# Kernel tuning notes

Hardware: AMD Instinct MI355X
Metric: run time of the kernel (lower is better)

## Reference

```python
import jax, jax.numpy as jnp
import numpy as np

B, T, N, F_IN, F_OUT, H = 32, 32, 256, 32, 32, 256
NEG_SLOPE = 0.2  # GATConv default leaky-relu slope


def setup_inputs() -> dict:
    key = jax.random.key(0)
    ks = jax.random.split(key, 12)
    x = jax.random.normal(ks[0], (B, T, N, F_IN), dtype=jnp.float32)
    u = jax.random.uniform(ks[1], (B, T, N, N))
    w = jax.random.uniform(ks[2], (B, T, N, N))
    adj = jnp.where(u < 0.1, w, 0.0).astype(jnp.float32)
    # GAT params (heads=1, concat=False)
    W = jax.random.normal(ks[3], (F_IN, F_OUT), dtype=jnp.float32) / np.sqrt(F_IN)
    a_src = jax.random.normal(ks[4], (F_OUT,), dtype=jnp.float32) / np.sqrt(F_OUT)
    a_dst = jax.random.normal(ks[5], (F_OUT,), dtype=jnp.float32) / np.sqrt(F_OUT)
    gat_b = jnp.zeros((F_OUT,), dtype=jnp.float32)
    # LSTM params (PyTorch layout, gate order i,f,g,o)
    IN = N * F_OUT
    s = 1.0 / np.sqrt(H)
    W_ih = jax.random.uniform(ks[6], (4 * H, IN), minval=-s, maxval=s, dtype=jnp.float32)
    W_hh = jax.random.uniform(ks[7], (4 * H, H), minval=-s, maxval=s, dtype=jnp.float32)
    b_ih = jax.random.uniform(ks[8], (4 * H,), minval=-s, maxval=s, dtype=jnp.float32)
    b_hh = jax.random.uniform(ks[9], (4 * H,), minval=-s, maxval=s, dtype=jnp.float32)
    # output Linear
    Wo = jax.random.uniform(ks[10], (N, H), minval=-s, maxval=s, dtype=jnp.float32)
    bo = jax.random.uniform(ks[11], (N,), minval=-s, maxval=s, dtype=jnp.float32)
    return {"x": x, "adj": adj, "W": W, "a_src": a_src, "a_dst": a_dst,
            "gat_b": gat_b, "W_ih": W_ih, "W_hh": W_hh, "b_ih": b_ih,
            "b_hh": b_hh, "Wo": Wo, "bo": bo}


def _gat(x, adj, W, a_src, a_dst, gat_b):
    # batched over (B,T). h: [B,T,N,F_OUT]
    h = jnp.einsum('btnf,fo->btno', x, W)
    s_src = jnp.einsum('btno,o->btn', h, a_src)  # contribution of source node j
    s_dst = jnp.einsum('btno,o->btn', h, a_dst)  # contribution of target node i
    # e[i,j] = LeakyReLU(a_dst.h_i + a_src.h_j)
    e = jax.nn.leaky_relu(s_dst[..., :, None] + s_src[..., None, :], NEG_SLOPE)
    # edge (row=j -> col=i) exists iff adj[j,i] != 0; GATConv adds self-loops
    mask = (jnp.swapaxes(adj, -1, -2) != 0) | jnp.eye(N, dtype=bool)
    alpha = jax.nn.softmax(jnp.where(mask, e, -jnp.inf), axis=-1)  # softmax over sources j per target i
    return jnp.einsum('btij,btjo->btio', alpha, h) + gat_b


def _lstm_last(seq, W_ih, W_hh, b_ih, b_hh):
    # seq: [B,T,IN] -> last hidden state [B,H]
    def step(carry, x_t):
        h_prev, c_prev = carry
        gates = x_t @ W_ih.T + h_prev @ W_hh.T + (b_ih + b_hh)
        i, f, g, o = jnp.split(gates, 4, axis=-1)
        c = jax.nn.sigmoid(f) * c_prev + jax.nn.sigmoid(i) * jnp.tanh(g)
        h = jax.nn.sigmoid(o) * jnp.tanh(c)
        return (h, c), None
    init = (jnp.zeros((seq.shape[0], H), seq.dtype), jnp.zeros((seq.shape[0], H), seq.dtype))
    (h_last, _), _ = jax.lax.scan(step, init, jnp.swapaxes(seq, 0, 1))
    return h_last


def reference(x, adj, W, a_src, a_dst, gat_b, W_ih, W_hh, b_ih, b_hh, Wo, bo):
    gat_out = _gat(x, adj, W, a_src, a_dst, gat_b)            # [B,T,N,F_OUT]
    seq = gat_out.reshape(gat_out.shape[0], gat_out.shape[1], -1)  # [B,T,N*F_OUT]
    h_last = _lstm_last(seq, W_ih, W_hh, b_ih, b_hh)          # [B,H]
    return h_last @ Wo.T + bo                                  # [B,N]
```

## Files before the change

### kernel.cpp

```cpp
#include <hip/hip_runtime.h>
#include <cstdint>

constexpr int B_ = 32, T_ = 32, N_ = 256, FIN = 32, FOUT = 32, H_ = 256;
constexpr int IN_ = N_ * FOUT;
constexpr int G4  = 4 * H_;
constexpr int BT  = B_ * T_;
#define NEG_SLOPE 0.2f

typedef _Float16 half8 __attribute__((ext_vector_type(8)));
typedef _Float16 h2    __attribute__((ext_vector_type(2)));
typedef float    f4    __attribute__((ext_vector_type(4)));

union U48 { uint4 u; half8 h; };

__device__ inline uint32_t pkh2(float a, float b) {
    union { uint32_t u; _Float16 h[2]; } z;
    z.h[0] = (_Float16)a; z.h[1] = (_Float16)b; return z.u;
}
__device__ inline float f16lo(uint32_t u){ union{uint32_t u; _Float16 h[2];} z; z.u=u; return (float)z.h[0]; }
__device__ inline float f16hi(uint32_t u){ union{uint32_t u; _Float16 h[2];} z; z.u=u; return (float)z.h[1]; }

__device__ inline float dot2f(uint32_t w, uint32_t h, float acc) {
    union { uint32_t u; h2 v; } a, b; a.u = w; b.u = h;
#if __has_builtin(__builtin_amdgcn_fdot2)
    return __builtin_amdgcn_fdot2(a.v, b.v, acc, false);
#else
    return acc + (float)a.v.x * (float)b.v.x + (float)a.v.y * (float)b.v.y;
#endif
}

__device__ inline void gload16(const void* g, void* l) {
    __builtin_amdgcn_global_load_lds(
        (const __attribute__((address_space(1))) void*)g,
        (__attribute__((address_space(3))) void*)l, 16, 0, 0);
}

__global__ __launch_bounds__(256) void gat_kernel(
    const float* __restrict__ x, const float* __restrict__ adj,
    const float* __restrict__ W, const float* __restrict__ a_src,
    const float* __restrict__ a_dst, const float* __restrict__ gat_b,
    _Float16* __restrict__ seq)
{
    const int bt = blockIdx.x;
    const int i  = threadIdx.x;
    const int L  = i & 63, w = i >> 6;
    __shared__ float Ws[FIN * FOUT];
    __shared__ __align__(16) _Float16 hT[32 * 264];
    __shared__ __align__(16) uint32_t Pc[256 * 36];
    __shared__ float ssrc[N_];
    __shared__ float linv[N_];
    __shared__ float asv[FOUT], adv[FOUT], gbv[FOUT];

    for (int t = i; t < FIN * FOUT; t += 256) Ws[t] = W[t];
    if (i < FOUT) { asv[i] = a_src[i]; adv[i] = a_dst[i]; gbv[i] = gat_b[i]; }

    float xr[FIN];
    const float* xrow = x + ((size_t)bt * N_ + i) * FIN;
    #pragma unroll
    for (int f4i = 0; f4i < FIN / 4; ++f4i) {
        float4 v = reinterpret_cast<const float4*>(xrow)[f4i];
        xr[4*f4i] = v.x; xr[4*f4i+1] = v.y; xr[4*f4i+2] = v.z; xr[4*f4i+3] = v.w;
    }
    __syncthreads();

    float hr[FOUT];
    #pragma unroll
    for (int k4 = 0; k4 < FOUT / 4; ++k4) {
        float ax = 0.f, ay = 0.f, az = 0.f, aw = 0.f;
        #pragma unroll
        for (int f = 0; f < FIN; ++f) {
            float4 w4 = *reinterpret_cast<const float4*>(&Ws[f*FOUT + 4*k4]);
            ax += xr[f]*w4.x; ay += xr[f]*w4.y; az += xr[f]*w4.z; aw += xr[f]*w4.w;
        }
        hr[4*k4] = ax; hr[4*k4+1] = ay; hr[4*k4+2] = az; hr[4*k4+3] = aw;
    }
    float ss = 0.f, sd = 0.f;
    #pragma unroll
    for (int k = 0; k < FOUT; ++k) { ss += hr[k]*asv[k]; sd += hr[k]*adv[k]; }
    #pragma unroll
    for (int k = 0; k < FOUT; ++k) hT[k*264 + i] = (_Float16)hr[k];
    ssrc[i] = ss;
    __syncthreads();

    float l = 0.f;
    f4 acc[4][2] = {};
    const float* adjcol = adj + (size_t)bt * N_ * N_ + i;
    const int key = (i >> 3) & 3;
    const int m = L & 15, G = L >> 4;

    for (int c = 0; c < 4; ++c) {
        const int j0 = c * 64;
        #pragma unroll 8
        for (int q = 0; q < 32; ++q) {
            int ja = j0 + 2*q, jb = ja + 1;
            float a0 = adjcol[(size_t)ja * N_];
            float a1 = adjcol[(size_t)jb * N_];
            float e0 = sd + ssrc[ja]; e0 = e0 > 0.f ? e0 : NEG_SLOPE * e0;
            float e1 = sd + ssrc[jb]; e1 = e1 > 0.f ? e1 : NEG_SLOPE * e1;
            float p0 = ((a0 != 0.f) || (ja == i)) ? __expf(e0) : 0.f;
            float p1 = ((a1 != 0.f) || (jb == i)) ? __expf(e1) : 0.f;
            l += p0 + p1;
            Pc[i*36 + (((q >> 2) ^ key) << 2) + (q & 3)] = pkh2(p0, p1);
        }
        #pragma unroll
        for (int ks = 0; ks < 2; ++ks) {
            U48 b0, b1;
            b0.h = *reinterpret_cast<const half8*>(&hT[m*264        + j0 + ks*32 + G*8]);
            b1.h = *reinterpret_cast<const half8*>(&hT[(m+16)*264   + j0 + ks*32 + G*8]);
            #pragma unroll
            for (int it = 0; it < 4; ++it) {
                int row = w*64 + it*16 + m;
                int rkey = (row >> 3) & 3;
                U48 a;
                a.u = reinterpret_cast<const uint4*>(&Pc[row*36])[ks*4 + (G ^ rkey)];
                acc[it][0] = __builtin_amdgcn_mfma_f32_16x16x32_f16(a.h, b0.h, acc[it][0], 0, 0, 0);
                acc[it][1] = __builtin_amdgcn_mfma_f32_16x16x32_f16(a.h, b1.h, acc[it][1], 0, 0, 0);
            }
        }
    }
    linv[i] = 1.f / l;
    _Float16* obase = seq + (size_t)bt * IN_;
    #pragma unroll
    for (int it = 0; it < 4; ++it) {
        int ib = w*64 + it*16 + G*4;
        #pragma unroll
        for (int ot = 0; ot < 2; ++ot) {
            int o = ot*16 + m;
            float gb = gbv[o];
            #pragma unroll
            for (int r = 0; r < 4; ++r) {
                int row = ib + r;
                obase[row * FOUT + o] = (_Float16)(acc[it][ot][r] * linv[row] + gb);
            }
        }
    }
}

__global__ __launch_bounds__(256) void pack_wih_kernel(
    const float* __restrict__ Wih, _Float16* __restrict__ out)
{
    int idx = (blockIdx.x * 256 + threadIdx.x) * 8;
    float4 v0 = *reinterpret_cast<const float4*>(Wih + idx);
    float4 v1 = *reinterpret_cast<const float4*>(Wih + idx + 4);
    half8 o;
    o[0]=(_Float16)v0.x; o[1]=(_Float16)v0.y; o[2]=(_Float16)v0.z; o[3]=(_Float16)v0.w;
    o[4]=(_Float16)v1.x; o[5]=(_Float16)v1.y; o[6]=(_Float16)v1.z; o[7]=(_Float16)v1.w;
    *reinterpret_cast<half8*>(out + idx) = o;
}

__global__ __launch_bounds__(256) void pack_whh_kernel(
    const float* __restrict__ Whh, uint32_t* __restrict__ pwv,
    uint32_t* __restrict__ pwl, uint32_t* __restrict__ pws)
{
    int g = blockIdx.x * 256 + threadIdx.x;
    const float* row = Whh + (size_t)g * H_;
    #pragma unroll
    for (int p = 0; p < 128; ++p) {
        float2 v = *reinterpret_cast<const float2*>(row + 2*p);
        uint32_t u = pkh2(v.x, v.y);
        if (p < 64) pwv[p * 1024 + g] = u;
        else if (p < 96) { int pp = p - 64; pwl[(pp >> 2) * 4096 + g * 4 + (pp & 3)] = u; }
        else             { int pp = p - 96; pws[(pp >> 2) * 4096 + g * 4 + (pp & 3)] = u; }
    }
}

__global__ __launch_bounds__(256, 4) void gemm_kernel(
    const _Float16* __restrict__ A, const _Float16* __restrict__ Bh,
    float* __restrict__ G)
{
    __shared__ __align__(16) _Float16 As[128 * 32];
    __shared__ __align__(16) _Float16 Bs[128 * 32];
    const int t = threadIdx.x;
    const int L = t & 63, w = t >> 6;
    const int wm = w & 1, wn = w >> 1;
    const int m0 = blockIdx.y * 128, n0 = blockIdx.x * 128;
    const int kz = blockIdx.z * 1024;

    f4 acc[4][4] = {};
    const int q0 = t, q1 = t + 256;
    const int row0 = q0 >> 2, kc0 = q0 & 3;
    const int row1 = q1 >> 2, kc1 = q1 & 3;
    const int la = (L & 15) * 32 + (L >> 4) * 8;

    const _Float16* A0 = A + (size_t)(m0 + row0) * IN_ + kz + kc0 * 8;
    const _Float16* A1 = A + (size_t)(m0 + row1) * IN_ + kz + kc1 * 8;
    const _Float16* B0 = Bh + (size_t)(n0 + row0) * IN_ + kz + kc0 * 8;
    const _Float16* B1 = Bh + (size_t)(n0 + row1) * IN_ + kz + kc1 * 8;
    for (int kb = 0; kb < 1024; kb += 32) {
        __syncthreads();
        gload16(A0 + kb, &As[q0 * 8]);
        gload16(A1 + kb, &As[q1 * 8]);
        gload16(B0 + kb, &Bs[q0 * 8]);
        gload16(B1 + kb, &Bs[q1 * 8]);
        __syncthreads();
        half8 af[4], bf[4];
        #pragma unroll
        for (int mi = 0; mi < 4; ++mi)
            af[mi] = *reinterpret_cast<const half8*>(&As[(wm*64 + mi*16) * 32 + la]);
        #pragma unroll
        for (int ni = 0; ni < 4; ++ni)
            bf[ni] = *reinterpret_cast<const half8*>(&Bs[(wn*64 + ni*16) * 32 + la]);
        #pragma unroll
        for (int mi = 0; mi < 4; ++mi)
            #pragma unroll
            for (int ni = 0; ni < 4; ++ni)
                acc[mi][ni] = __builtin_amdgcn_mfma_f32_16x16x32_f16(
                    af[mi], bf[ni], acc[mi][ni], 0, 0, 0);
    }
    const int cn = n0 + wn * 64 + (L & 15);
    const int rm = m0 + wm * 64 + (L >> 4) * 4;
    #pragma unroll
    for (int mi = 0; mi < 4; ++mi)
        #pragma unroll
        for (int ni = 0; ni < 4; ++ni)
            #pragma unroll
            for (int r = 0; r < 4; ++r)
                atomicAdd(&G[(size_t)(rm + mi*16 + r) * G4 + cn + ni*16], acc[mi][ni][r]);
}

__global__ __launch_bounds__(1024) void lstm_kernel(
    const float* __restrict__ G, const uint32_t* __restrict__ pwv,
    const uint32_t* __restrict__ pwl, const uint32_t* __restrict__ pws,
    const float* __restrict__ b_ih, const float* __restrict__ b_hh,
    const float* __restrict__ Wo, const float* __restrict__ bo,
    float* __restrict__ out)
{
    const int b = blockIdx.x;
    const int g = threadIdx.x;
    __shared__ __align__(16) uint32_t hsp[128];
    __shared__ float gsh[G4];
    __shared__ __align__(16) uint32_t wl[8 * 4096];

    uint32_t wv[64];
    #pragma unroll
    for (int p = 0; p < 64; ++p) wv[p] = pwv[p * 1024 + g];
    {
        const uint4* s = reinterpret_cast<const uint4*>(pwl);
        uint4* d = reinterpret_cast<uint4*>(wl);
        #pragma unroll
        for (int r = 0; r < 8; ++r) d[r * 1024 + g] = s[r * 1024 + g];
    }
    if (g < 128) hsp[g] = 0u;
    float c = 0.f;
    const float bias = b_ih[g] + b_hh[g];
    const float* Gb = G + (size_t)b * T_ * G4 + g;
    const uint4* pws4 = reinterpret_cast<const uint4*>(pws);
    const uint4* wl4  = reinterpret_cast<const uint4*>(wl);
    const uint4* hsp4 = reinterpret_cast<const uint4*>(hsp);
    float gnext = Gb[0];
    __syncthreads();

    for (int t = 0; t < T_; ++t) {
        float acc = bias + gnext;
        if (t + 1 < T_) gnext = Gb[(size_t)(t + 1) * G4];
        #pragma unroll
        for (int q = 0; q < 32; ++q) {
            uint4 h4 = hsp4[q];
            uint4 w4;
            if (q < 16) {
                w4.x = wv[4*q]; w4.y = wv[4*q+1]; w4.z = wv[4*q+2]; w4.w = wv[4*q+3];
            } else if (q < 24) {
                w4 = wl4[(q - 16) * 1024 + g];
            } else {
                w4 = pws4[(q - 24) * 1024 + g];
            }
            acc = dot2f(w4.x, h4.x, acc);
            acc = dot2f(w4.y, h4.y, acc);
            acc = dot2f(w4.z, h4.z, acc);
            acc = dot2f(w4.w, h4.w, acc);
        }
        gsh[g] = acc;
        __syncthreads();
        if (g < H_) {
            float xi = gsh[g], xf = gsh[H_ + g], xg = gsh[2*H_ + g], xo = gsh[3*H_ + g];
            float si = 1.f / (1.f + __expf(-xi));
            float sf = 1.f / (1.f + __expf(-xf));
            float so = 1.f / (1.f + __expf(-xo));
            float eg = __expf(2.f * xg);
            float tg = 1.f - 2.f / (eg + 1.f);
            c = sf * c + si * tg;
            float ec = __expf(2.f * c);
            float th = 1.f - 2.f / (ec + 1.f);
            reinterpret_cast<_Float16*>(hsp)[g] = (_Float16)(so * th);
        }
        __syncthreads();
    }
    if (g < N_) {
        const float* worow = Wo + (size_t)g * H_;
        float o = bo[g];
        #pragma unroll
        for (int q = 0; q < 32; ++q) {
            uint4 hq = hsp4[q];
            float4 w0 = *reinterpret_cast<const float4*>(worow + q*8);
            float4 w1 = *reinterpret_cast<const float4*>(worow + q*8 + 4);
            o += w0.x * f16lo(hq.x) + w0.y * f16hi(hq.x)
               + w0.z * f16lo(hq.y) + w0.w * f16hi(hq.y)
               + w1.x * f16lo(hq.z) + w1.y * f16hi(hq.z)
               + w1.z * f16lo(hq.w) + w1.w * f16hi(hq.w);
        }
        out[(size_t)b * N_ + g] = o;
    }
}

extern "C" void kernel_launch(void* const* d_in, const int* in_sizes, int n_in,
                              void* d_out, int out_size, void* d_ws, size_t ws_size,
                              hipStream_t stream) {
    const float* x     = (const float*)d_in[0];
    const float* adj   = (const float*)d_in[1];
    const float* W     = (const float*)d_in[2];
    const float* a_src = (const float*)d_in[3];
    const float* a_dst = (const float*)d_in[4];
    const float* gat_b = (const float*)d_in[5];
    const float* W_ih  = (const float*)d_in[6];
    const float* W_hh  = (const float*)d_in[7];
    const float* b_ih  = (const float*)d_in[8];
    const float* b_hh  = (const float*)d_in[9];
    const float* Wo    = (const float*)d_in[10];
    const float* bo    = (const float*)d_in[11];
    float* out = (float*)d_out;

    _Float16* seq   = (_Float16*)d_ws;
    _Float16* wih_h = seq + (size_t)BT * IN_;
    float*    G     = (float*)(wih_h + (size_t)G4 * IN_);
    uint32_t* pwv   = (uint32_t*)(G + (size_t)BT * G4);
    uint32_t* pwl   = pwv + 64 * 1024;
    uint32_t* pws   = pwl + 32 * 1024;

    hipMemsetAsync(G, 0, (size_t)BT * G4 * sizeof(float), stream);
    pack_whh_kernel<<<dim3(4), dim3(256), 0, stream>>>(W_hh, pwv, pwl, pws);
    pack_wih_kernel<<<dim3(4096), dim3(256), 0, stream>>>(W_ih, wih_h);
    gat_kernel<<<dim3(BT), dim3(256), 0, stream>>>(x, adj, W, a_src, a_dst, gat_b, seq);
    gemm_kernel<<<dim3(8, 8, 8), dim3(256), 0, stream>>>(seq, wih_h, G);
    lstm_kernel<<<dim3(B_), dim3(1024), 0, stream>>>(G, pwv, pwl, pws, b_ih, b_hh, Wo, bo, out);
}
```

Measured before the change: 585.0 us.

## Replace split-K atomics with partial buffers reduced in LSTM; merge pack kernels

Each split-K slice of the input-projection GEMM now writes its own partial buffer instead of doing atomicAdd into one shared buffer. The LSTM kernel sums the eight partials while it prefetches the next timestep's gates. This removes the memset and the atomic traffic. The two weight-packing kernels are merged into one launch. The cost is eight times the workspace for the partials and more global reads inside the serial LSTM loop.

```diff
diff --git a/kernel.cpp b/kernel.cpp
--- a/kernel.cpp
+++ b/kernel.cpp
@@ -5,6 +5,7 @@
 constexpr int IN_ = N_ * FOUT;
 constexpr int G4  = 4 * H_;
 constexpr int BT  = B_ * T_;
+constexpr int KZ  = 8;
 #define NEG_SLOPE 0.2f
 
 typedef _Float16 half8 __attribute__((ext_vector_type(8)));
@@ -105,8 +106,8 @@
         #pragma unroll
         for (int ks = 0; ks < 2; ++ks) {
             U48 b0, b1;
-            b0.h = *reinterpret_cast<const half8*>(&hT[m*264        + j0 + ks*32 + G*8]);
-            b1.h = *reinterpret_cast<const half8*>(&hT[(m+16)*264   + j0 + ks*32 + G*8]);
+            b0.h = *reinterpret_cast<const half8*>(&hT[m*264      + j0 + ks*32 + G*8]);
+            b1.h = *reinterpret_cast<const half8*>(&hT[(m+16)*264 + j0 + ks*32 + G*8]);
             #pragma unroll
             for (int it = 0; it < 4; ++it) {
                 int row = w*64 + it*16 + m;
@@ -136,37 +137,36 @@
     }
 }
 
-__global__ __launch_bounds__(256) void pack_wih_kernel(
-    const float* __restrict__ Wih, _Float16* __restrict__ out)
-{
-    int idx = (blockIdx.x * 256 + threadIdx.x) * 8;
-    float4 v0 = *reinterpret_cast<const float4*>(Wih + idx);
-    float4 v1 = *reinterpret_cast<const float4*>(Wih + idx + 4);
-    half8 o;
-    o[0]=(_Float16)v0.x; o[1]=(_Float16)v0.y; o[2]=(_Float16)v0.z; o[3]=(_Float16)v0.w;
-    o[4]=(_Float16)v1.x; o[5]=(_Float16)v1.y; o[6]=(_Float16)v1.z; o[7]=(_Float16)v1.w;
-    *reinterpret_cast<half8*>(out + idx) = o;
-}
-
-__global__ __launch_bounds__(256) void pack_whh_kernel(
-    const float* __restrict__ Whh, uint32_t* __restrict__ pwv,
+__global__ __launch_bounds__(256) void pack_kernel(
+    const float* __restrict__ Wih, const float* __restrict__ Whh,
+    _Float16* __restrict__ wih_h, uint32_t* __restrict__ pwv,
     uint32_t* __restrict__ pwl, uint32_t* __restrict__ pws)
 {
-    int g = blockIdx.x * 256 + threadIdx.x;
-    const float* row = Whh + (size_t)g * H_;
-    #pragma unroll
-    for (int p = 0; p < 128; ++p) {
-        float2 v = *reinterpret_cast<const float2*>(row + 2*p);
-        uint32_t u = pkh2(v.x, v.y);
-        if (p < 64) pwv[p * 1024 + g] = u;
-        else if (p < 96) { int pp = p - 64; pwl[(pp >> 2) * 4096 + g * 4 + (pp & 3)] = u; }
-        else             { int pp = p - 96; pws[(pp >> 2) * 4096 + g * 4 + (pp & 3)] = u; }
+    if (blockIdx.x < 4096) {
+        int idx = (blockIdx.x * 256 + threadIdx.x) * 8;
+        float4 v0 = *reinterpret_cast<const float4*>(Wih + idx);
+        float4 v1 = *reinterpret_cast<const float4*>(Wih + idx + 4);
+        half8 o;
+        o[0]=(_Float16)v0.x; o[1]=(_Float16)v0.y; o[2]=(_Float16)v0.z; o[3]=(_Float16)v0.w;
+        o[4]=(_Float16)v1.x; o[5]=(_Float16)v1.y; o[6]=(_Float16)v1.z; o[7]=(_Float16)v1.w;
+        *reinterpret_cast<half8*>(wih_h + idx) = o;
+    } else {
+        int g = (blockIdx.x - 4096) * 256 + threadIdx.x;
+        const float* row = Whh + (size_t)g * H_;
+        #pragma unroll
+        for (int p = 0; p < 128; ++p) {
+            float2 v = *reinterpret_cast<const float2*>(row + 2*p);
+            uint32_t u = pkh2(v.x, v.y);
+            if (p < 64) pwv[p * 1024 + g] = u;
+            else if (p < 96) { int pp = p - 64; pwl[(pp >> 2) * 4096 + g * 4 + (pp & 3)] = u; }
+            else             { int pp = p - 96; pws[(pp >> 2) * 4096 + g * 4 + (pp & 3)] = u; }
+        }
     }
 }
 
 __global__ __launch_bounds__(256, 4) void gemm_kernel(
     const _Float16* __restrict__ A, const _Float16* __restrict__ Bh,
-    float* __restrict__ G)
+    float* __restrict__ Gp)
 {
     __shared__ __align__(16) _Float16 As[128 * 32];
     __shared__ __align__(16) _Float16 Bs[128 * 32];
@@ -207,6 +207,7 @@
                 acc[mi][ni] = __builtin_amdgcn_mfma_f32_16x16x32_f16(
                     af[mi], bf[ni], acc[mi][ni], 0, 0, 0);
     }
+    float* Gz = Gp + (size_t)blockIdx.z * BT * G4;
     const int cn = n0 + wn * 64 + (L & 15);
     const int rm = m0 + wm * 64 + (L >> 4) * 4;
     #pragma unroll
@@ -215,11 +216,11 @@
         for (int ni = 0; ni < 4; ++ni)
             #pragma unroll
             for (int r = 0; r < 4; ++r)
-                atomicAdd(&G[(size_t)(rm + mi*16 + r) * G4 + cn + ni*16], acc[mi][ni][r]);
+                Gz[(size_t)(rm + mi*16 + r) * G4 + cn + ni*16] = acc[mi][ni][r];
 }
 
 __global__ __launch_bounds__(1024) void lstm_kernel(
-    const float* __restrict__ G, const uint32_t* __restrict__ pwv,
+    const float* __restrict__ Gp, const uint32_t* __restrict__ pwv,
     const uint32_t* __restrict__ pwl, const uint32_t* __restrict__ pws,
     const float* __restrict__ b_ih, const float* __restrict__ b_hh,
     const float* __restrict__ Wo, const float* __restrict__ bo,
@@ -243,16 +244,23 @@
     if (g < 128) hsp[g] = 0u;
     float c = 0.f;
     const float bias = b_ih[g] + b_hh[g];
-    const float* Gb = G + (size_t)b * T_ * G4 + g;
+    const size_t zs = (size_t)BT * G4;
+    const float* Gb = Gp + (size_t)b * T_ * G4 + g;
     const uint4* pws4 = reinterpret_cast<const uint4*>(pws);
     const uint4* wl4  = reinterpret_cast<const uint4*>(wl);
     const uint4* hsp4 = reinterpret_cast<const uint4*>(hsp);
-    float gnext = Gb[0];
+
+    float gcur = 0.f;
+    #pragma unroll
+    for (int z = 0; z < KZ; ++z) gcur += Gb[z * zs];
     __syncthreads();
 
     for (int t = 0; t < T_; ++t) {
-        float acc = bias + gnext;
-        if (t + 1 < T_) gnext = Gb[(size_t)(t + 1) * G4];
+        float acc = bias + gcur;
+        float pf[KZ];
+        const int tn = (t + 1 < T_) ? t + 1 : t;
+        #pragma unroll
+        for (int z = 0; z < KZ; ++z) pf[z] = Gb[(size_t)tn * G4 + z * zs];
         #pragma unroll
         for (int q = 0; q < 32; ++q) {
             uint4 h4 = hsp4[q];
@@ -269,6 +277,7 @@
             acc = dot2f(w4.z, h4.z, acc);
             acc = dot2f(w4.w, h4.w, acc);
         }
+        gcur = ((pf[0]+pf[1]) + (pf[2]+pf[3])) + ((pf[4]+pf[5]) + (pf[6]+pf[7]));
         gsh[g] = acc;
         __syncthreads();
         if (g < H_) {
@@ -321,15 +330,13 @@
 
     _Float16* seq   = (_Float16*)d_ws;
     _Float16* wih_h = seq + (size_t)BT * IN_;
-    float*    G     = (float*)(wih_h + (size_t)G4 * IN_);
-    uint32_t* pwv   = (uint32_t*)(G + (size_t)BT * G4);
+    float*    Gp    = (float*)(wih_h + (size_t)G4 * IN_);
+    uint32_t* pwv   = (uint32_t*)(Gp + (size_t)KZ * BT * G4);
     uint32_t* pwl   = pwv + 64 * 1024;
     uint32_t* pws   = pwl + 32 * 1024;
 
-    hipMemsetAsync(G, 0, (size_t)BT * G4 * sizeof(float), stream);
-    pack_whh_kernel<<<dim3(4), dim3(256), 0, stream>>>(W_hh, pwv, pwl, pws);
-    pack_wih_kernel<<<dim3(4096), dim3(256), 0, stream>>>(W_ih, wih_h);
+    pack_kernel<<<dim3(4100), dim3(256), 0, stream>>>(W_ih, W_hh, wih_h, pwv, pwl, pws);
     gat_kernel<<<dim3(BT), dim3(256), 0, stream>>>(x, adj, W, a_src, a_dst, gat_b, seq);
-    gemm_kernel<<<dim3(8, 8, 8), dim3(256), 0, stream>>>(seq, wih_h, G);
-    lstm_kernel<<<dim3(B_), dim3(1024), 0, stream>>>(G, pwv, pwl, pws, b_ih, b_hh, Wo, bo, out);
-}
+    gemm_kernel<<<dim3(8, 8, KZ), dim3(256), 0, stream>>>(seq, wih_h, Gp);
+    lstm_kernel<<<dim3(B_), dim3(1024), 0, stream>>>(Gp, pwv, pwl, pws, b_ih, b_hh, Wo, bo, out);
+}
```

Measured after the change: 569.8 us. 2.6% less time.
